# Kernel tuning notes

Hardware: AMD Instinct MI355X
Metric: run time of the kernel (lower is better)

Reference implementation:

```python
import jax, jax.numpy as jnp
import numpy as np

D_MODEL = 768
NHEAD = 12
HEAD_DIM = D_MODEL // NHEAD
B, L = 8, 1024


def setup_inputs() -> dict:
    key = jax.random.key(0)
    ks = jax.random.split(key, 10)
    s = 0.02  # init scale for weights
    return {
        "x": jax.random.normal(ks[0], (B, L, D_MODEL), dtype=jnp.float32),
        "pos": jax.random.normal(ks[1], (B, L, D_MODEL), dtype=jnp.float32),
        "qkv_w": jax.random.normal(ks[2], (3 * D_MODEL, D_MODEL), dtype=jnp.float32) * s,
        "qkv_b": jnp.zeros((3 * D_MODEL,), dtype=jnp.float32),
        "pq_w": jax.random.normal(ks[3], (D_MODEL, D_MODEL), dtype=jnp.float32) * s,
        "pq_b": jnp.zeros((D_MODEL,), dtype=jnp.float32),
        "pk_w": jax.random.normal(ks[4], (D_MODEL, D_MODEL), dtype=jnp.float32) * s,
        "pk_b": jnp.zeros((D_MODEL,), dtype=jnp.float32),
    }


def reference(x, pos, qkv_w, qkv_b, pq_w, pq_b, pk_w, pk_b):
    b, l, d = x.shape
    h, hd = NHEAD, HEAD_DIM

    qkv = x @ qkv_w.T + qkv_b  # (b, l, 3d)
    q, k, v = jnp.split(qkv, 3, axis=-1)
    # rearrange 'b l (h d) -> b l h d'
    q = q.reshape(b, l, h, hd)
    k = k.reshape(b, l, h, hd)
    v = v.reshape(b, l, h, hd)

    pq = (pos @ pq_w.T + pq_b).reshape(b, l, h, hd)
    pk = (pos @ pk_w.T + pk_b).reshape(b, l, h, hd)

    CC = jnp.einsum('bnhd,blhd->bhnl', q, k)
    CP = jnp.einsum('bnhd,blhd->bhnl', q, pq)
    PC = jnp.einsum('bnhd,blhd->bhnl', k, pk)

    # Faithful to source: only PC is scaled (operator precedence in original)
    scale = (3 * d) ** 0.5
    attn = jax.nn.softmax(CC + CP + PC / scale, axis=-1)

    out = jnp.einsum('bhnl,blhd->bnhd', attn, v)  # (b, n, h, hd)
    return out
```

## Files before the change

### kernel.cpp

```cpp
#include <hip/hip_runtime.h>
#include <hip/hip_bf16.h>

#define NHEAD 12
#define BATCH 8
#define SEQ 1024
#define LOG2E 1.4426950408889634f

typedef __bf16 bf16x8 __attribute__((ext_vector_type(8)));
typedef float  f32x4  __attribute__((ext_vector_type(4)));

#define WAITVM0 asm volatile("s_waitcnt vmcnt(0)" ::: "memory")

#define MFMA(A, B, C) __builtin_amdgcn_mfma_f32_16x16x32_bf16(A, B, C, 0, 0, 0)

__device__ __forceinline__ unsigned short f2bf(float f) {
    union { float f; unsigned u; } v; v.f = f;
    unsigned u = v.u;
    u += 0x7fff + ((u >> 16) & 1);
    return (unsigned short)(u >> 16);
}

__device__ __forceinline__ unsigned pkbf(float a, float b) {
    union { __hip_bfloat162 h; unsigned u; } cv;
    cv.h = __float22bfloat162_rn(make_float2(a, b));
    return cv.u;
}

__device__ __forceinline__ void gload_lds16(const void* g, void* l) {
    __builtin_amdgcn_global_load_lds(
        (const __attribute__((address_space(1))) unsigned*)g,
        (__attribute__((address_space(3))) unsigned*)l, 16, 0, 0);
}

#define SZ_X    6291456
#define SZ_QKVW 1769472
#define SZ_PW   589824
#define CONV_TOTAL 15532032

__global__ __launch_bounds__(256) void convert_kernel(
    const float* __restrict__ x, const float* __restrict__ pos,
    const float* __restrict__ qkv_w, const float* __restrict__ pq_w,
    const float* __restrict__ pk_w, unsigned short* __restrict__ dst)
{
    const size_t i4 = ((size_t)blockIdx.x * 256 + threadIdx.x) * 4;
    if (i4 >= CONV_TOTAL) return;
    const float* src; size_t off;
    if (i4 < SZ_X)                { src = x;     off = i4; }
    else if (i4 < 2 * SZ_X)       { src = pos;   off = i4 - SZ_X; }
    else if (i4 < 2 * SZ_X + SZ_QKVW) { src = qkv_w; off = i4 - 2 * SZ_X; }
    else if (i4 < 2 * SZ_X + SZ_QKVW + SZ_PW) { src = pq_w; off = i4 - 2 * SZ_X - SZ_QKVW; }
    else                          { src = pk_w;  off = i4 - 2 * SZ_X - SZ_QKVW - SZ_PW; }
    float4 v = *(const float4*)(src + off);
    ushort4 o;
    o.x = f2bf(v.x); o.y = f2bf(v.y); o.z = f2bf(v.z); o.w = f2bf(v.w);
    *(ushort4*)(dst + i4) = o;
}


#define PROJ_STAGE(K0, AS, BS) do {                                          \
    const int k0_ = (K0);                                                    \
    const unsigned short* asrc_; int acol_;                                  \
    if (g == 4)                    { asrc_ = posb; acol_ = k0_; }            \
    else if (g == 3 && k0_ >= 768) { asrc_ = posb; acol_ = k0_ - 768; }      \
    else                           { asrc_ = xb;   acol_ = k0_; }            \
    gload_lds16(asrc_ + (size_t)(m0 + r0) * 768 + acol_ + q0 * 8, &AS[base0]);\
    gload_lds16(asrc_ + (size_t)(m0 + r1) * 768 + acol_ + q1 * 8, &AS[base1]);\
    const unsigned short* wsrc_; int wro_, wco_;                             \
    if (g <= 2)       { wsrc_ = qkvw; wro_ = n0;        wco_ = k0_; }        \
    else if (g == 3) {                                                       \
        if (k0_ < 768) { wsrc_ = qkvw; wro_ = n0 - 1536; wco_ = k0_; }       \
        else           { wsrc_ = pqw;  wro_ = n0 - 2304; wco_ = k0_ - 768; } \
    } else            { wsrc_ = pkw;  wro_ = n0 - 3072; wco_ = k0_; }        \
    gload_lds16(wsrc_ + (size_t)(wro_ + r0) * 768 + wco_ + q0 * 8, &BS[base0]);\
    gload_lds16(wsrc_ + (size_t)(wro_ + r1) * 768 + wco_ + q1 * 8, &BS[base1]);\
} while (0)

#define PROJ_COMPUTE(AS, BS) do {                                            \
    bf16x8 af[4], bfr[4];                                                    \
    _Pragma("unroll")                                                        \
    for (int mt = 0; mt < 4; ++mt) {                                         \
        const int rr = wm + mt * 16 + col16;                                 \
        af[mt] = *(const bf16x8*)&AS[rr * 32 + ((quad ^ ((rr >> 1) & 3)) * 8)];\
    }                                                                        \
    _Pragma("unroll")                                                        \
    for (int nt = 0; nt < 4; ++nt) {                                         \
        const int rr = wn + nt * 16 + col16;                                 \
        bfr[nt] = *(const bf16x8*)&BS[rr * 32 + ((quad ^ ((rr >> 1) & 3)) * 8)];\
    }                                                                        \
    _Pragma("unroll")                                                        \
    for (int mt = 0; mt < 4; ++mt)                                           \
        _Pragma("unroll")                                                    \
        for (int nt = 0; nt < 4; ++nt)                                       \
            acc[mt][nt] = MFMA(af[mt], bfr[nt], acc[mt][nt]);                \
} while (0)

__global__ __launch_bounds__(256, 3) void proj_kernel(
    const unsigned short* __restrict__ xb, const unsigned short* __restrict__ posb,
    const unsigned short* __restrict__ qkvw, const unsigned short* __restrict__ pqw,
    const unsigned short* __restrict__ pkw,
    const float* __restrict__ qkv_b, const float* __restrict__ pq_b,
    const float* __restrict__ pk_b,
    unsigned short* __restrict__ Q2, unsigned short* __restrict__ K2,
    unsigned short* __restrict__ Vt, int band)
{
    __shared__ unsigned short As0[128 * 32];
    __shared__ unsigned short As1[128 * 32];
    __shared__ unsigned short Bs0[128 * 32];
    __shared__ unsigned short Bs1[128 * 32];

    const int id  = blockIdx.x;
    const int xcd = id & 7;
    const int idx = id >> 3;
    const int nt30 = (idx / band + 18) % 30;
    const int m0 = (xcd * band + idx % band) * 128;
    const int n0 = nt30 * 128;
    const int g  = n0 / 768;
    const int nk = (g == 3) ? 48 : 24;

    const int tid   = threadIdx.x;
    const int lane  = tid & 63;
    const int w     = tid >> 6;
    const int wm    = (w & 1) * 64;
    const int wn    = (w >> 1) * 64;
    const int quad  = lane >> 4;
    const int col16 = lane & 15;

    const int c0 = w * 64 + lane;
    const int c1 = c0 + 256;
    const int r0 = c0 >> 2, q0 = (c0 & 3) ^ ((c0 >> 3) & 3);
    const int r1 = c1 >> 2, q1 = (c1 & 3) ^ ((c1 >> 3) & 3);
    const int base0 = (w * 64) * 8;
    const int base1 = (w * 64 + 256) * 8;

    f32x4 acc[4][4];
    const f32x4 fzero = {0.f, 0.f, 0.f, 0.f};
#pragma unroll
    for (int mt = 0; mt < 4; ++mt)
#pragma unroll
        for (int nt = 0; nt < 4; ++nt) acc[mt][nt] = fzero;

    PROJ_STAGE(0, As0, Bs0);

    for (int kt = 0; kt < nk; kt += 2) {
        WAITVM0;
        __syncthreads();
        PROJ_STAGE((kt + 1) * 32, As1, Bs1);
        PROJ_COMPUTE(As0, Bs0);

        WAITVM0;
        __syncthreads();
        if (kt + 2 < nk) PROJ_STAGE((kt + 2) * 32, As0, Bs0);
        PROJ_COMPUTE(As1, Bs1);
    }

#pragma unroll
    for (int mt = 0; mt < 4; ++mt) {
        const int mbase = m0 + wm + mt * 16 + quad * 4;
#pragma unroll
        for (int nt = 0; nt < 4; ++nt) {
            const int n = n0 + wn + nt * 16 + col16;
            if (g == 2) {
                const int b = mbase >> 10, l0 = mbase & 1023;
                const int c = n - 1536, h = c >> 6, dd = c & 63;
                const float bias = qkv_b[n];
                uint2 pk;
                pk.x = pkbf(acc[mt][nt][0] + bias, acc[mt][nt][1] + bias);
                pk.y = pkbf(acc[mt][nt][2] + bias, acc[mt][nt][3] + bias);
                *(uint2*)&Vt[((size_t)(b * NHEAD + h) * 64 + dd) * 1024 + l0] = pk;
                continue;
            }
#pragma unroll
            for (int r = 0; r < 4; ++r) {
                const int m = mbase + r;
                const int b = m >> 10, l = m & 1023;
                float val = acc[mt][nt][r];
                if (g == 0) {
                    val = (val + qkv_b[n]) * LOG2E;
                    const int h = n >> 6, dd = n & 63;
                    Q2[((size_t)(b * NHEAD + h) * 1024 + l) * 128 + dd] = f2bf(val);
                } else if (g == 1) {
                    val = (val + qkv_b[n]) * (LOG2E / 48.0f);
                    const int c = n - 768, h = c >> 6, dd = c & 63;
                    Q2[((size_t)(b * NHEAD + h) * 1024 + l) * 128 + 64 + dd] = f2bf(val);
                } else if (g == 3) {
                    const int c = n - 2304;
                    val += qkv_b[n - 1536] + pq_b[c];
                    const int h = c >> 6, dd = c & 63;
                    K2[((size_t)(b * NHEAD + h) * 1024 + l) * 128 + dd] = f2bf(val);
                } else {
                    const int c = n - 3072;
                    val += pk_b[c];
                    const int h = c >> 6, dd = c & 63;
                    K2[((size_t)(b * NHEAD + h) * 1024 + l) * 128 + 64 + dd] = f2bf(val);
                }
            }
        }
    }
}


#define ATTN_STG(J0, KS, VS) do {                                            \
    const int j0_ = (J0);                                                    \
    gload_lds16(&K2[q2base + (size_t)(j0_ + kr0) * 128 + kc0 * 8], &KS[kbase0]);\
    gload_lds16(&K2[q2base + (size_t)(j0_ + kr1) * 128 + kc1 * 8], &KS[kbase1]);\
    gload_lds16(&Vt[vtbase + (size_t)vr * 1024 + j0_ + vc * 8],    &VS[vbase]);\
} while (0)

#define ATTN_PV(VS, PSR) do {                                                \
    bf16x8 bp0 = *(const bf16x8*)&PSR[w][col16][quad * 8];                   \
    bf16x8 bp1 = *(const bf16x8*)&PSR[w][16 + col16][quad * 8];              \
    _Pragma("unroll")                                                        \
    for (int c2 = 0; c2 < 4; ++c2) {                                         \
        const int rv = c2 * 16 + col16;                                      \
        bf16x8 av = *(const bf16x8*)&VS[rv * 32 + ((quad ^ ((rv >> 2) & 3)) * 8)];\
        o[0][c2] = MFMA(av, bp0, o[0][c2]);                                  \
        o[1][c2] = MFMA(av, bp1, o[1][c2]);                                  \
    }                                                                        \
} while (0)

#define ATTN_QK(KS, PSW) do {                                                \
    f32x4 st[2][2] = {{fzero, fzero}, {fzero, fzero}};                       \
    _Pragma("unroll")                                                        \
    for (int kk = 0; kk < 4; ++kk) {                                         \
        const int rrj0 = col16, rrj1 = 16 + col16;                           \
        bf16x8 kf0 = *(const bf16x8*)&KS[rrj0 * 128 + (((kk * 4 + quad) ^ (rrj0 & 15)) * 8)];\
        bf16x8 kf1 = *(const bf16x8*)&KS[rrj1 * 128 + (((kk * 4 + quad) ^ (rrj1 & 15)) * 8)];\
        _Pragma("unroll")                                                    \
        for (int qt = 0; qt < 2; ++qt) {                                     \
            st[0][qt] = MFMA(kf0, bq[qt][kk], st[0][qt]);                    \
            st[1][qt] = MFMA(kf1, bq[qt][kk], st[1][qt]);                    \
        }                                                                    \
    }                                                                        \
    _Pragma("unroll")                                                        \
    for (int qt = 0; qt < 2; ++qt) {                                         \
        float p0[4], p1[4], s = 0.f;                                         \
        _Pragma("unroll")                                                    \
        for (int r = 0; r < 4; ++r) {                                        \
            p0[r] = __builtin_amdgcn_exp2f(st[0][qt][r]);                    \
            p1[r] = __builtin_amdgcn_exp2f(st[1][qt][r]);                    \
            s += p0[r] + p1[r];                                              \
        }                                                                    \
        lsum[qt] += s;                                                       \
        uint2 w0, w1;                                                        \
        w0.x = pkbf(p0[0], p0[1]); w0.y = pkbf(p0[2], p0[3]);                \
        w1.x = pkbf(p1[0], p1[1]); w1.y = pkbf(p1[2], p1[3]);                \
        *(uint2*)&PSW[w][qt * 16 + col16][quad * 4]      = w0;               \
        *(uint2*)&PSW[w][qt * 16 + col16][16 + quad * 4] = w1;               \
    }                                                                        \
} while (0)

#define ATTN_PHASE(J, KQK, KST, VPV, VST, PSW, PSR, DOPV, DOST) do {         \
    WAITVM0;                                                                 \
    __syncthreads();                                                         \
    if (DOST) ATTN_STG(((J) + 1) * 32, KST, VST);                            \
    if (DOPV) ATTN_PV(VPV, PSR);                                             \
    ATTN_QK(KQK, PSW);                                                       \
} while (0)

__global__ __launch_bounds__(256, 3) void attn_kernel(
    const unsigned short* __restrict__ Q2, const unsigned short* __restrict__ K2,
    const unsigned short* __restrict__ Vt, float* __restrict__ out, int b0)
{
    __shared__ unsigned short K2sA[32 * 128];
    __shared__ unsigned short K2sB[32 * 128];
    __shared__ unsigned short VtX[64 * 32];
    __shared__ unsigned short VtY[64 * 32];
    __shared__ unsigned short VtZ[64 * 32];
    __shared__ unsigned short Ps0[4][32][40];
    __shared__ unsigned short Ps1[4][32][40];

    const int bh_l = blockIdx.x;
    const int b = b0 + bh_l / NHEAD, h = bh_l % NHEAD;
    const int tid   = threadIdx.x;
    const int lane  = tid & 63;
    const int w     = tid >> 6;
    const int quad  = lane >> 4;
    const int col16 = lane & 15;
    const int qbase = blockIdx.y * 128 + w * 32;

    const size_t q2base = (size_t)bh_l * 1024 * 128;
    const size_t vtbase = (size_t)bh_l * 64 * 1024;

    const int kL0 = w * 64 + lane, kL1 = kL0 + 256;
    const int kr0 = kL0 >> 4, kc0 = (kL0 & 15) ^ (kr0 & 15);
    const int kr1 = kL1 >> 4, kc1 = (kL1 & 15) ^ (kr1 & 15);
    const int vL  = w * 64 + lane;
    const int vr  = vL >> 2,  vc  = (vL & 3) ^ ((vL >> 4) & 3);
    const int kbase0 = (w * 64) * 8, kbase1 = (w * 64 + 256) * 8;
    const int vbase  = (w * 64) * 8;

    bf16x8 bq[2][4];
#pragma unroll
    for (int qt = 0; qt < 2; ++qt)
#pragma unroll
        for (int kk = 0; kk < 4; ++kk)
            bq[qt][kk] = *(const bf16x8*)&Q2[q2base +
                (size_t)(qbase + qt * 16 + col16) * 128 + kk * 32 + quad * 8];

    f32x4 o[2][4];
    const f32x4 fzero = {0.f, 0.f, 0.f, 0.f};
#pragma unroll
    for (int qt = 0; qt < 2; ++qt)
#pragma unroll
        for (int c2 = 0; c2 < 4; ++c2) o[qt][c2] = fzero;
    float lsum[2] = {0.f, 0.f};

    ATTN_STG(0, K2sA, VtX);

    ATTN_PHASE(0, K2sA, K2sB, VtZ, VtY, Ps0, Ps1, 0, 1);

    for (int j = 1; j < 31; j += 6) {
        ATTN_PHASE(j + 0, K2sB, K2sA, VtX, VtZ, Ps1, Ps0, 1, 1);
        ATTN_PHASE(j + 1, K2sA, K2sB, VtY, VtX, Ps0, Ps1, 1, 1);
        ATTN_PHASE(j + 2, K2sB, K2sA, VtZ, VtY, Ps1, Ps0, 1, 1);
        ATTN_PHASE(j + 3, K2sA, K2sB, VtX, VtZ, Ps0, Ps1, 1, 1);
        ATTN_PHASE(j + 4, K2sB, K2sA, VtY, VtX, Ps1, Ps0, 1, 1);
        ATTN_PHASE(j + 5, K2sA, K2sB, VtZ, VtY, Ps0, Ps1, 1, 1);
    }

    ATTN_PHASE(31, K2sB, K2sA, VtX, VtZ, Ps1, Ps0, 1, 0);

    ATTN_PV(VtY, Ps1);

#pragma unroll
    for (int qt = 0; qt < 2; ++qt) {
        lsum[qt] += __shfl_xor(lsum[qt], 16, 64);
        lsum[qt] += __shfl_xor(lsum[qt], 32, 64);
    }

#pragma unroll
    for (int qt = 0; qt < 2; ++qt) {
        const float inv = 1.0f / lsum[qt];
        const int q = qbase + qt * 16 + col16;
#pragma unroll
        for (int c2 = 0; c2 < 4; ++c2) {
#pragma unroll
            for (int r = 0; r < 4; ++r) {
                const int dd = c2 * 16 + quad * 4 + r;
                out[(((size_t)(b * 1024 + q)) * 12 + h) * 64 + dd] = o[qt][c2][r] * inv;
            }
        }
    }
}

extern "C" void kernel_launch(void* const* d_in, const int* in_sizes, int n_in,
                              void* d_out, int out_size, void* d_ws, size_t ws_size,
                              hipStream_t stream) {
    const float* x     = (const float*)d_in[0];
    const float* pos   = (const float*)d_in[1];
    const float* qkv_w = (const float*)d_in[2];
    const float* qkv_b = (const float*)d_in[3];
    const float* pq_w  = (const float*)d_in[4];
    const float* pq_b  = (const float*)d_in[5];
    const float* pk_w  = (const float*)d_in[6];
    const float* pk_b  = (const float*)d_in[7];
    float* out = (float*)d_out;

    unsigned short* ws   = (unsigned short*)d_ws;
    unsigned short* xb   = ws;
    unsigned short* posb = xb + SZ_X;
    unsigned short* qkvw = posb + SZ_X;
    unsigned short* pqw  = qkvw + SZ_QKVW;
    unsigned short* pkw  = pqw + SZ_PW;
    unsigned short* cbuf = pkw + SZ_PW;

    const size_t conv_bytes = (size_t)CONV_TOTAL * 2;
    const size_t per_batch  = (size_t)NHEAD * 1024 * 128 * 4
                            + (size_t)NHEAD * 64 * 1024 * 2;
    int cb = BATCH;
    while (cb > 1 && conv_bytes + (size_t)cb * per_batch > ws_size) cb >>= 1;

    unsigned short* Q2 = cbuf;
    unsigned short* K2 = Q2 + (size_t)cb * NHEAD * 1024 * 128;
    unsigned short* Vt = K2 + (size_t)cb * NHEAD * 1024 * 128;

    convert_kernel<<<(CONV_TOTAL / 4 + 255) / 256, 256, 0, stream>>>(
        x, pos, qkv_w, pq_w, pk_w, ws);

    for (int b0 = 0; b0 < BATCH; b0 += cb) {
        proj_kernel<<<dim3(cb * 240), 256, 0, stream>>>(
            xb + (size_t)b0 * 1024 * 768, posb + (size_t)b0 * 1024 * 768,
            qkvw, pqw, pkw, qkv_b, pq_b, pk_b, Q2, K2, Vt, cb);
        attn_kernel<<<dim3(cb * NHEAD, 8), 256, 0, stream>>>(Q2, K2, Vt, out, b0);
    }
}
```

Measured before the change: 240.9 us.

## Triple-buffer projection GEMM loads and stage epilogue through LDS for vector stores

```diff
diff --git a/kernel.cpp b/kernel.cpp
--- a/kernel.cpp
+++ b/kernel.cpp
@@ -10,6 +10,7 @@
 typedef float  f32x4  __attribute__((ext_vector_type(4)));
 
 #define WAITVM0 asm volatile("s_waitcnt vmcnt(0)" ::: "memory")
+#define WAITVM4 asm volatile("s_waitcnt vmcnt(4)" ::: "memory")
 
 #define MFMA(A, B, C) __builtin_amdgcn_mfma_f32_16x16x32_bf16(A, B, C, 0, 0, 0)
 
@@ -105,8 +106,10 @@
 {
     __shared__ unsigned short As0[128 * 32];
     __shared__ unsigned short As1[128 * 32];
+    __shared__ unsigned short As2[128 * 32];
     __shared__ unsigned short Bs0[128 * 32];
     __shared__ unsigned short Bs1[128 * 32];
+    __shared__ unsigned short Bs2[128 * 32];
 
     const int id  = blockIdx.x;
     const int xcd = id & 7;
@@ -140,26 +143,32 @@
         for (int nt = 0; nt < 4; ++nt) acc[mt][nt] = fzero;
 
     PROJ_STAGE(0, As0, Bs0);
-
-    for (int kt = 0; kt < nk; kt += 2) {
-        WAITVM0;
+    PROJ_STAGE(32, As1, Bs1);
+
+    for (int kt = 0; kt < nk; kt += 3) {
+        WAITVM4;
         __syncthreads();
-        PROJ_STAGE((kt + 1) * 32, As1, Bs1);
+        PROJ_STAGE((kt + 2) * 32, As2, Bs2);
         PROJ_COMPUTE(As0, Bs0);
 
-        WAITVM0;
+        WAITVM4;
         __syncthreads();
-        if (kt + 2 < nk) PROJ_STAGE((kt + 2) * 32, As0, Bs0);
+        if (kt + 3 < nk) PROJ_STAGE((kt + 3) * 32, As0, Bs0);
         PROJ_COMPUTE(As1, Bs1);
-    }
-
-#pragma unroll
-    for (int mt = 0; mt < 4; ++mt) {
-        const int mbase = m0 + wm + mt * 16 + quad * 4;
-#pragma unroll
-        for (int nt = 0; nt < 4; ++nt) {
-            const int n = n0 + wn + nt * 16 + col16;
-            if (g == 2) {
+
+        if (kt + 3 >= nk) { WAITVM0; } else { WAITVM4; }
+        __syncthreads();
+        if (kt + 4 < nk) PROJ_STAGE((kt + 4) * 32, As1, Bs1);
+        PROJ_COMPUTE(As2, Bs2);
+    }
+
+    if (g == 2) {
+#pragma unroll
+        for (int mt = 0; mt < 4; ++mt) {
+            const int mbase = m0 + wm + mt * 16 + quad * 4;
+#pragma unroll
+            for (int nt = 0; nt < 4; ++nt) {
+                const int n = n0 + wn + nt * 16 + col16;
                 const int b = mbase >> 10, l0 = mbase & 1023;
                 const int c = n - 1536, h = c >> 6, dd = c & 63;
                 const float bias = qkv_b[n];
@@ -167,32 +176,53 @@
                 pk.x = pkbf(acc[mt][nt][0] + bias, acc[mt][nt][1] + bias);
                 pk.y = pkbf(acc[mt][nt][2] + bias, acc[mt][nt][3] + bias);
                 *(uint2*)&Vt[((size_t)(b * NHEAD + h) * 64 + dd) * 1024 + l0] = pk;
-                continue;
             }
-#pragma unroll
-            for (int r = 0; r < 4; ++r) {
-                const int m = mbase + r;
+        }
+    } else {
+#pragma unroll
+        for (int p = 0; p < 4; ++p) {
+            __syncthreads();
+            if ((wm >> 6) == (p >> 1)) {
+#pragma unroll
+                for (int mth = 0; mth < 2; ++mth) {
+                    const int mt = ((p & 1) << 1) | mth;
+#pragma unroll
+                    for (int nt = 0; nt < 4; ++nt) {
+                        const int n = n0 + wn + nt * 16 + col16;
+                        float badd, bmul;
+                        if (g == 0)      { badd = qkv_b[n];                         bmul = LOG2E; }
+                        else if (g == 1) { badd = qkv_b[n];                         bmul = LOG2E / 48.0f; }
+                        else if (g == 3) { badd = qkv_b[n - 1536] + pq_b[n - 2304]; bmul = 1.0f; }
+                        else             { badd = pk_b[n - 3072];                   bmul = 1.0f; }
+                        const int lrb  = mth * 16 + quad * 4;
+                        const int ccol = wn + nt * 16 + col16;
+#pragma unroll
+                        for (int r = 0; r < 4; ++r)
+                            As0[(lrb + r) * 128 + ccol] =
+                                f2bf((acc[mt][nt][r] + badd) * bmul);
+                    }
+                }
+            }
+            __syncthreads();
+#pragma unroll
+            for (int j = 0; j < 2; ++j) {
+                const int u = tid + 256 * j;
+                const int rowp = u >> 4;
+                const int seg  = u & 15;
+                const int m = m0 + p * 32 + rowp;
                 const int b = m >> 10, l = m & 1023;
-                float val = acc[mt][nt][r];
-                if (g == 0) {
-                    val = (val + qkv_b[n]) * LOG2E;
-                    const int h = n >> 6, dd = n & 63;
-                    Q2[((size_t)(b * NHEAD + h) * 1024 + l) * 128 + dd] = f2bf(val);
-                } else if (g == 1) {
-                    val = (val + qkv_b[n]) * (LOG2E / 48.0f);
-                    const int c = n - 768, h = c >> 6, dd = c & 63;
-                    Q2[((size_t)(b * NHEAD + h) * 1024 + l) * 128 + 64 + dd] = f2bf(val);
-                } else if (g == 3) {
-                    const int c = n - 2304;
-                    val += qkv_b[n - 1536] + pq_b[c];
-                    const int h = c >> 6, dd = c & 63;
-                    K2[((size_t)(b * NHEAD + h) * 1024 + l) * 128 + dd] = f2bf(val);
-                } else {
-                    const int c = n - 3072;
-                    val += pk_b[c];
-                    const int h = c >> 6, dd = c & 63;
-                    K2[((size_t)(b * NHEAD + h) * 1024 + l) * 128 + 64 + dd] = f2bf(val);
-                }
+                const int n = n0 + seg * 8;
+                uint4 v = *(const uint4*)&As0[rowp * 128 + seg * 8];
+                unsigned short* dst;
+                if (g == 0)      { const int h = n >> 6, dd = n & 63;
+                                   dst = &Q2[((size_t)(b * NHEAD + h) * 1024 + l) * 128 + dd]; }
+                else if (g == 1) { const int c = n - 768,  h = c >> 6, dd = c & 63;
+                                   dst = &Q2[((size_t)(b * NHEAD + h) * 1024 + l) * 128 + 64 + dd]; }
+                else if (g == 3) { const int c = n - 2304, h = c >> 6, dd = c & 63;
+                                   dst = &K2[((size_t)(b * NHEAD + h) * 1024 + l) * 128 + dd]; }
+                else             { const int c = n - 3072, h = c >> 6, dd = c & 63;
+                                   dst = &K2[((size_t)(b * NHEAD + h) * 1024 + l) * 128 + 64 + dd]; }
+                *(uint4*)dst = v;
             }
         }
     }
```

After: 234.1 us. 1.03x faster.
